# Kernel tuning notes

Hardware: AMD Instinct MI355X
Metric: run time of the kernel (lower is better)

The kernel has to match this reference:

```python
import jax, jax.numpy as jnp
import numpy as np

TEMPERATURE = 0.1


def setup_inputs() -> dict:
    key = jax.random.key(0)
    k1, k2 = jax.random.split(key)
    pred = jax.random.normal(k1, (4, 64, 32), dtype=jnp.float32)
    target = jax.random.normal(k2, (4, 64, 32), dtype=jnp.float32)
    return {"pred": pred, "target": target}


def reference(pred, target):
    # All inputs are finite and no mask is given, so valid_both is all-True and
    # the torch boolean flatten pred[valid_both] is exactly a reshape(-1).
    p = pred.reshape(-1)
    t = target.reshape(-1)
    n = p.shape[0]  # 8192
    # diff[i, j] = x[j] - x[i]; product is symmetric so orientation is irrelevant.
    pd = p[None, :] - p[:, None]           # [n, n]
    td = t[None, :] - t[:, None]           # [n, n]
    agreement = jnp.tanh(pd * td / TEMPERATURE)
    # mean over strict upper triangle (i < j): mask-and-sum, divide by pair count.
    upper = jnp.triu(jnp.ones((n, n), dtype=agreement.dtype), k=1)
    n_pairs = jnp.asarray(n * (n - 1) // 2, dtype=agreement.dtype)
    tau = jnp.sum(agreement * upper) / n_pairs
    return tau
```

## Files before the change

kernel.cpp:

```cpp
#include <hip/hip_runtime.h>


#define NTOT 8192
#define JBLK 16
#define NBLK (NTOT / JBLK)
#define TPB  256
#define KPT  (NTOT / TPB)

#if __has_builtin(__builtin_amdgcn_exp2f)
#define FAST_EXP2(x) __builtin_amdgcn_exp2f(x)
#else
#define FAST_EXP2(x) exp2f(x)
#endif
#if __has_builtin(__builtin_amdgcn_rcpf)
#define FAST_RCP(x) __builtin_amdgcn_rcpf(x)
#else
#define FAST_RCP(x) (1.0f / (x))
#endif

__global__ __launch_bounds__(TPB) void ktau_partial(const float* __restrict__ pred,
                                                    const float* __restrict__ targ,
                                                    double* __restrict__ partial) {
    const float C = 28.853900817779268f;

    __shared__ float sp[JBLK];
    __shared__ float st[JBLK];
    __shared__ double red[TPB];

    const int tid = threadIdx.x;
    const int j0  = blockIdx.x * JBLK;

    if (tid < JBLK) {
        sp[tid] = pred[j0 + tid];
        st[tid] = targ[j0 + tid] * C;
    }

    float pi[KPT], ti[KPT];
#pragma unroll
    for (int k = 0; k < KPT; ++k) {
        const int i = tid + k * TPB;
        pi[k] = pred[i];
        ti[k] = targ[i] * C;
    }
    __syncthreads();

    double dacc = 0.0;
#pragma unroll 2
    for (int j = 0; j < JBLK; ++j) {
        const float pj = sp[j];
        const float tj = st[j];
        float facc = 0.0f;
#pragma unroll
        for (int k = 0; k < KPT; ++k) {
            const float x = (pi[k] - pj) * (ti[k] - tj);
            const float e = FAST_EXP2(x);
            const float r = FAST_RCP(e + 1.0f);
            facc = __builtin_fmaf(-2.0f, r, facc);
        }
        dacc += (double)facc;
    }
    dacc += (double)(JBLK * KPT);

    red[tid] = dacc;
    __syncthreads();
    for (int s = TPB / 2; s > 0; s >>= 1) {
        if (tid < s) red[tid] += red[tid + s];
        __syncthreads();
    }
    if (tid == 0) partial[blockIdx.x] = red[0];
}

__global__ __launch_bounds__(NBLK) void ktau_final(const double* __restrict__ partial,
                                                   float* __restrict__ out) {
    __shared__ double red[NBLK];
    const int tid = threadIdx.x;
    red[tid] = partial[tid];
    __syncthreads();
    for (int s = NBLK / 2; s > 0; s >>= 1) {
        if (tid < s) red[tid] += red[tid + s];
        __syncthreads();
    }
    if (tid == 0) {
        const double n_ordered_pairs = (double)NTOT * (double)(NTOT - 1);
        out[0] = (float)(red[0] / n_ordered_pairs);
    }
}

extern "C" void kernel_launch(void* const* d_in, const int* in_sizes, int n_in,
                              void* d_out, int out_size, void* d_ws, size_t ws_size,
                              hipStream_t stream) {
    const float* pred = (const float*)d_in[0];
    const float* targ = (const float*)d_in[1];
    float* out = (float*)d_out;
    double* partial = (double*)d_ws;

    ktau_partial<<<NBLK, TPB, 0, stream>>>(pred, targ, partial);
    ktau_final<<<1, NBLK, 0, stream>>>(partial, out);
}
```

Baseline: 74.71 us.

## Register-block j values, swap loop order, use wave-shuffle reductions

```diff
diff --git a/kernel.cpp b/kernel.cpp
--- a/kernel.cpp
+++ b/kernel.cpp
@@ -2,37 +2,23 @@
 
 
 #define NTOT 8192
-#define JBLK 16
+#define TPB  512
+#define KPT  (NTOT / TPB)
+#define JBLK 8
 #define NBLK (NTOT / JBLK)
-#define TPB  256
-#define KPT  (NTOT / TPB)
-
-#if __has_builtin(__builtin_amdgcn_exp2f)
-#define FAST_EXP2(x) __builtin_amdgcn_exp2f(x)
-#else
-#define FAST_EXP2(x) exp2f(x)
-#endif
-#if __has_builtin(__builtin_amdgcn_rcpf)
-#define FAST_RCP(x) __builtin_amdgcn_rcpf(x)
-#else
-#define FAST_RCP(x) (1.0f / (x))
-#endif
 
 __global__ __launch_bounds__(TPB) void ktau_partial(const float* __restrict__ pred,
                                                     const float* __restrict__ targ,
                                                     double* __restrict__ partial) {
     const float C = 28.853900817779268f;
-
-    __shared__ float sp[JBLK];
-    __shared__ float st[JBLK];
-    __shared__ double red[TPB];
-
     const int tid = threadIdx.x;
     const int j0  = blockIdx.x * JBLK;
 
-    if (tid < JBLK) {
-        sp[tid] = pred[j0 + tid];
-        st[tid] = targ[j0 + tid] * C;
+    float pj[JBLK], tj[JBLK];
+#pragma unroll
+    for (int jj = 0; jj < JBLK; ++jj) {
+        pj[jj] = pred[j0 + jj];
+        tj[jj] = targ[j0 + jj] * C;
     }
 
     float pi[KPT], ti[KPT];
@@ -42,47 +28,56 @@
         pi[k] = pred[i];
         ti[k] = targ[i] * C;
     }
+
+    float acc[JBLK];
+#pragma unroll
+    for (int jj = 0; jj < JBLK; ++jj) acc[jj] = 0.0f;
+
+#pragma unroll 2
+    for (int k = 0; k < KPT; ++k) {
+#pragma unroll
+        for (int jj = 0; jj < JBLK; ++jj) {
+            const float x = (pi[k] - pj[jj]) * (ti[k] - tj[jj]);
+            const float e = __builtin_amdgcn_exp2f(x);
+            const float r = __builtin_amdgcn_rcpf(e + 1.0f);
+            acc[jj] = __builtin_fmaf(-2.0f, r, acc[jj]);
+        }
+    }
+
+    float fsum = 0.0f;
+#pragma unroll
+    for (int jj = 0; jj < JBLK; ++jj) fsum += acc[jj];
+
+    double dacc = (double)fsum;
+#pragma unroll
+    for (int off = 32; off > 0; off >>= 1)
+        dacc += __shfl_down(dacc, off, 64);
+
+    __shared__ double red[TPB / 64];
+    const int wave = tid >> 6;
+    if ((tid & 63) == 0) red[wave] = dacc;
     __syncthreads();
-
-    double dacc = 0.0;
-#pragma unroll 2
-    for (int j = 0; j < JBLK; ++j) {
-        const float pj = sp[j];
-        const float tj = st[j];
-        float facc = 0.0f;
+    if (tid == 0) {
+        double s = 0.0;
 #pragma unroll
-        for (int k = 0; k < KPT; ++k) {
-            const float x = (pi[k] - pj) * (ti[k] - tj);
-            const float e = FAST_EXP2(x);
-            const float r = FAST_RCP(e + 1.0f);
-            facc = __builtin_fmaf(-2.0f, r, facc);
-        }
-        dacc += (double)facc;
+        for (int w = 0; w < TPB / 64; ++w) s += red[w];
+        partial[blockIdx.x] = s + (double)(TPB * KPT * JBLK);
     }
-    dacc += (double)(JBLK * KPT);
-
-    red[tid] = dacc;
-    __syncthreads();
-    for (int s = TPB / 2; s > 0; s >>= 1) {
-        if (tid < s) red[tid] += red[tid + s];
-        __syncthreads();
-    }
-    if (tid == 0) partial[blockIdx.x] = red[0];
 }
 
-__global__ __launch_bounds__(NBLK) void ktau_final(const double* __restrict__ partial,
-                                                   float* __restrict__ out) {
-    __shared__ double red[NBLK];
+__global__ __launch_bounds__(256) void ktau_final(const double* __restrict__ partial,
+                                                  float* __restrict__ out) {
     const int tid = threadIdx.x;
-    red[tid] = partial[tid];
+    double s = partial[tid] + partial[tid + 256] + partial[tid + 512] + partial[tid + 768];
+#pragma unroll
+    for (int off = 32; off > 0; off >>= 1)
+        s += __shfl_down(s, off, 64);
+    __shared__ double red[4];
+    if ((tid & 63) == 0) red[tid >> 6] = s;
     __syncthreads();
-    for (int s = NBLK / 2; s > 0; s >>= 1) {
-        if (tid < s) red[tid] += red[tid + s];
-        __syncthreads();
-    }
     if (tid == 0) {
-        const double n_ordered_pairs = (double)NTOT * (double)(NTOT - 1);
-        out[0] = (float)(red[0] / n_ordered_pairs);
+        const double t = red[0] + red[1] + red[2] + red[3];
+        out[0] = (float)(t / ((double)NTOT * (double)(NTOT - 1)));
     }
 }
 
@@ -95,5 +90,5 @@
     double* partial = (double*)d_ws;
 
     ktau_partial<<<NBLK, TPB, 0, stream>>>(pred, targ, partial);
-    ktau_final<<<1, NBLK, 0, stream>>>(partial, out);
+    ktau_final<<<1, 256, 0, stream>>>(partial, out);
 }
```

Measured after the change: 71.44 us. 1.05x faster.
